# Kernel optimization log

Hardware: AMD Instinct MI355X
Metric: run time of the kernel (lower is better)

## Reference

```python
import jax, jax.numpy as jnp
import numpy as np

T, N, R = 10, 50000, 50000   # time steps, nodes per graph, total restaurants
D_IN, D, H = 128, 64, 4      # input dim, hidden dim, attention heads
E = 400000                   # edges per timestep (before self-loops)
HD = D // H                  # head dim


def setup_inputs() -> dict:
    key = jax.random.key(0)
    ks = jax.random.split(key, 16)
    inp = {}
    inp["x"] = jax.random.normal(ks[0], (T, N, D_IN), jnp.float32)
    inp["edge_index"] = jax.random.randint(ks[1], (T, 2, E), 0, N, jnp.int32)
    inp["edge_weight"] = jax.random.uniform(ks[2], (T, E), jnp.float32)
    # per-timestep permutation mapping local node idx -> global restaurant idx
    inp["global_idx"] = jax.vmap(lambda k: jax.random.permutation(k, R))(
        jax.random.split(ks[3], T)).astype(jnp.int32)
    s = 0.05
    inp["gcn1_w"] = jax.random.normal(ks[4], (D, D_IN), jnp.float32) * s
    inp["gcn1_b"] = jnp.zeros((D,), jnp.float32)
    inp["gcn2_w"] = jax.random.normal(ks[5], (D, D), jnp.float32) * s
    inp["gcn2_b"] = jnp.zeros((D,), jnp.float32)
    inp["in_proj_w"] = jax.random.normal(ks[6], (3 * D, D), jnp.float32) * s
    inp["in_proj_b"] = jnp.zeros((3 * D,), jnp.float32)
    inp["out_proj_w"] = jax.random.normal(ks[7], (D, D), jnp.float32) * s
    inp["out_proj_b"] = jnp.zeros((D,), jnp.float32)
    inp["w1"] = jnp.ones((T, D), jnp.float32)
    inp["w2"] = jnp.ones((T, D), jnp.float32)
    inp["w3"] = jnp.ones((D,), jnp.float32)
    inp["w4"] = jnp.ones((D,), jnp.float32)
    inp["ln1_g"] = jnp.ones((D,), jnp.float32)
    inp["ln1_b"] = jnp.zeros((D,), jnp.float32)
    inp["ln2_g"] = jnp.ones((D,), jnp.float32)
    inp["ln2_b"] = jnp.zeros((D,), jnp.float32)
    inp["fc_w"] = jax.random.normal(ks[8], (D, D), jnp.float32) * s
    inp["fc_b"] = jnp.zeros((D,), jnp.float32)
    return inp


def _layer_norm(x, g, b, eps=1e-5):
    mu = jnp.mean(x, axis=-1, keepdims=True)
    var = jnp.mean((x - mu) ** 2, axis=-1, keepdims=True)
    return (x - mu) * jax.lax.rsqrt(var + eps) * g + b


def _gcn_layer(h, src, dst, ew, W, b):
    # PyG GCNConv with edge weights; self-loops already appended by caller.
    deg = jax.ops.segment_sum(ew, dst, num_segments=N)
    dinv = jnp.where(deg > 0, jax.lax.rsqrt(deg), 0.0)
    norm = dinv[src] * ew * dinv[dst]                      # [E+N]
    hw = h @ W.T                                           # [N, D]
    agg = jax.ops.segment_sum(norm[:, None] * hw[src], dst, num_segments=N)
    return agg + b


def _forward(x, edge_index, edge_weight, global_idx,
             gcn1_w, gcn1_b, gcn2_w, gcn2_b,
             in_proj_w, in_proj_b, out_proj_w, out_proj_b,
             w1, w2, w3, w4, ln1_g, ln1_b, ln2_g, ln2_b, fc_w, fc_b):
    loop = jnp.arange(N, dtype=edge_index.dtype)
    src = jnp.concatenate([edge_index[:, 0], jnp.broadcast_to(loop, (T, N))], axis=1)
    dst = jnp.concatenate([edge_index[:, 1], jnp.broadcast_to(loop, (T, N))], axis=1)
    ew = jnp.concatenate([edge_weight, jnp.ones((T, N), edge_weight.dtype)], axis=1)

    def per_t(xt, st, dt, wt):
        h = jax.nn.relu(_gcn_layer(xt, st, dt, wt, gcn1_w, gcn1_b))
        return jax.nn.relu(_gcn_layer(h, st, dt, wt, gcn2_w, gcn2_b))

    feat = jax.vmap(per_t)(x, src, dst, ew)                # [T, N, D]

    # scatter local features to global alignment (permutation per timestep)
    aligned = jax.vmap(lambda g, f: jnp.zeros((R, D), f.dtype).at[g].set(f))(
        global_idx, feat)                                  # [T, R, D]
    time_embeds = jnp.transpose(aligned, (1, 0, 2))        # [R, T, D]

    presence = jax.vmap(
        lambda g: jnp.zeros((R,), bool).at[g].set(True))(global_idx)  # [T, R]
    key_padding_mask = ~presence.T                          # [R, T], True = ignore
    bias = jnp.where(key_padding_mask, -1e9, 0.0)           # [R, T]

    # multi-head self-attention over time axis (batch_first, batch = R)
    qkv = time_embeds @ in_proj_w.T + in_proj_b             # [R, T, 3D]
    q, k, v = jnp.split(qkv, 3, axis=-1)
    q = q.reshape(R, T, H, HD)
    k = k.reshape(R, T, H, HD)
    v = v.reshape(R, T, H, HD)
    scores = jnp.einsum('rthd,rshd->rhts', q, k) / np.sqrt(HD)
    scores = scores + bias[:, None, None, :]
    attn = jax.nn.softmax(scores, axis=-1)                  # [R, H, T, T]
    ao = jnp.einsum('rhts,rshd->rthd', attn, v).reshape(R, T, D)
    attn_out = ao @ out_proj_w.T + out_proj_b               # [R, T, D]

    # dropouts are identity in eval mode
    time_feat = _layer_norm(w1 * time_embeds + w2 * attn_out, ln1_g, ln1_b)
    final = time_feat[:, -1, :]                             # [R, D]
    out = final @ fc_w.T + fc_b                             # [R, D]
    return _layer_norm(w3 * final + w4 * out, ln2_g, ln2_b)


def reference(x, edge_index, edge_weight, global_idx,
              gcn1_w, gcn1_b, gcn2_w, gcn2_b,
              in_proj_w, in_proj_b, out_proj_w, out_proj_b,
              w1, w2, w3, w4, ln1_g, ln1_b, ln2_g, ln2_b, fc_w, fc_b):
    return _forward(x, edge_index, edge_weight, global_idx,
                    gcn1_w, gcn1_b, gcn2_w, gcn2_b,
                    in_proj_w, in_proj_b, out_proj_w, out_proj_b,
                    w1, w2, w3, w4, ln1_g, ln1_b, ln2_g, ln2_b, fc_w, fc_b)
```

## Files before the change

### kernel.cpp

```cpp
#include <hip/hip_runtime.h>
#include <cstdint>
#include <cstddef>

namespace {

constexpr int T = 10;
constexpr int N = 50000;
constexpr int R = 50000;
constexpr int DIN = 128;
constexpr int D = 64;
constexpr int E = 400000;

constexpr int BINS = 16384;
constexpr int NR = 4;
constexpr int SEG = 16;
constexpr int ESEG = E / SEG;
constexpr int EV4 = ESEG / 4;

constexpr float WSCALE = 262144.0f;
constexpr float WINV = 1.0f / 262144.0f;

typedef _Float16 h16;
typedef __attribute__((ext_vector_type(8))) _Float16 f16x8;
typedef __attribute__((ext_vector_type(4))) _Float16 f16x4;
typedef __attribute__((ext_vector_type(4))) float f32x4;

__global__ __launch_bounds__(256) void k_hist(const int* __restrict__ ei,
                                              const float* __restrict__ ew,
                                              unsigned* __restrict__ pu) {
  __shared__ unsigned h[BINS];
  int b = blockIdx.x;
  int s = b % SEG;
  int tr = b / SEG;
  int r = tr % NR;
  int t = tr / NR;
  for (int i = threadIdx.x; i < BINS; i += 256) h[i] = 0u;
  __syncthreads();
  int bin0 = r * BINS;
  const int4* dst4 = (const int4*)(ei + (size_t)t * 2 * E + E + s * ESEG);
  const float4* ew4 = (const float4*)(ew + (size_t)t * E + s * ESEG);
  for (int i = threadIdx.x; i < EV4; i += 256) {
    int4 d = dst4[i];
    float4 w = ew4[i];
    unsigned a0 = (unsigned)(d.x - bin0);
    unsigned a1 = (unsigned)(d.y - bin0);
    unsigned a2 = (unsigned)(d.z - bin0);
    unsigned a3 = (unsigned)(d.w - bin0);
    if (a0 < (unsigned)BINS) atomicAdd(&h[a0], 0x1000000u + (unsigned)fmaf(w.x, WSCALE, 0.5f));
    if (a1 < (unsigned)BINS) atomicAdd(&h[a1], 0x1000000u + (unsigned)fmaf(w.y, WSCALE, 0.5f));
    if (a2 < (unsigned)BINS) atomicAdd(&h[a2], 0x1000000u + (unsigned)fmaf(w.z, WSCALE, 0.5f));
    if (a3 < (unsigned)BINS) atomicAdd(&h[a3], 0x1000000u + (unsigned)fmaf(w.w, WSCALE, 0.5f));
  }
  __syncthreads();
  size_t base = (size_t)b * BINS;
  for (int i = threadIdx.x; i < BINS; i += 256) pu[base + i] = h[i];
}

__global__ __launch_bounds__(256) void k_hreduce(const unsigned* __restrict__ pu,
                                                 int* __restrict__ cnt,
                                                 float* __restrict__ dinv) {
  int i = blockIdx.x * 256 + threadIdx.x;
  if (i >= T * N) return;
  int t = i / N, n = i - t * N;
  int r = n / BINS, rel = n - r * BINS;
  unsigned c = 0;
  unsigned wsum = 0;
  #pragma unroll
  for (int s = 0; s < SEG; ++s) {
    unsigned v = pu[((size_t)((t * NR + r) * SEG + s)) * BINS + rel];
    c += v >> 24;
    wsum += v & 0xFFFFFFu;
  }
  cnt[i] = (int)c;
  dinv[i] = rsqrtf(1.0f + (float)wsum * WINV);
}

__global__ __launch_bounds__(256) void k_scan(const int* __restrict__ cnt,
                                              int* __restrict__ rowptr) {
  int t = blockIdx.x;
  int lane = threadIdx.x & 63, wid = threadIdx.x >> 6;
  __shared__ int wsum[4];
  __shared__ int carry_s;
  if (threadIdx.x == 0) carry_s = 0;
  __syncthreads();
  const int4* cp = (const int4*)(cnt + (size_t)t * N);
  int4* rp = (int4*)(rowptr + (size_t)t * N);
  constexpr int NI4 = N / 4;
  for (int base = 0; base < NI4; base += 256) {
    int i = base + threadIdx.x;
    int4 v = make_int4(0, 0, 0, 0);
    if (i < NI4) v = cp[i];
    int tot = v.x + v.y + v.z + v.w;
    int s = tot;
    #pragma unroll
    for (int off = 1; off < 64; off <<= 1) {
      int u = __shfl_up(s, off, 64);
      if (lane >= off) s += u;
    }
    if (lane == 63) wsum[wid] = s;
    int carry = carry_s;
    __syncthreads();
    int wadd = 0;
    #pragma unroll
    for (int w = 0; w < 4; ++w) if (w < wid) wadd += wsum[w];
    if (i < NI4) {
      int excl = carry + wadd + s - tot;
      int4 o;
      o.x = excl;
      o.y = excl + v.x;
      o.z = o.y + v.y;
      o.w = o.z + v.z;
      rp[i] = o;
    }
    __syncthreads();
    if (threadIdx.x == 0) carry_s = carry + wsum[0] + wsum[1] + wsum[2] + wsum[3];
    __syncthreads();
  }
}

__global__ __launch_bounds__(256) void k_segoff(unsigned* __restrict__ pu,
                                                const int* __restrict__ rowptr) {
  int i = blockIdx.x * 256 + threadIdx.x;
  if (i >= T * N) return;
  int t = i / N, n = i - t * N;
  int r = n / BINS, rel = n - r * BINS;
  unsigned run = (unsigned)rowptr[i];
  #pragma unroll
  for (int s = 0; s < SEG; ++s) {
    size_t base = ((size_t)((t * NR + r) * SEG + s)) * BINS + rel;
    unsigned v = pu[base];
    pu[base] = run;
    run += v >> 24;
  }
}

__global__ __launch_bounds__(256) void k_fill2(const int* __restrict__ ei,
                                               const float* __restrict__ ew,
                                               const unsigned* __restrict__ pu,
                                               int2* __restrict__ pk) {
  __shared__ int cur[BINS];
  int b = blockIdx.x;
  int s = b % SEG;
  int tr = b / SEG;
  int r = tr % NR;
  int t = tr / NR;
  size_t pbase = (size_t)b * BINS;
  for (int i = threadIdx.x; i < BINS; i += 256) cur[i] = (int)pu[pbase + i];
  __syncthreads();
  int bin0 = r * BINS;
  const int4* src4 = (const int4*)(ei + (size_t)t * 2 * E + s * ESEG);
  const int4* dst4 = (const int4*)(ei + (size_t)t * 2 * E + E + s * ESEG);
  const float4* ew4 = (const float4*)(ew + (size_t)t * E + s * ESEG);
  int2* pkt = pk + (size_t)t * E;
  for (int i = threadIdx.x; i < EV4; i += 256) {
    int4 d = dst4[i];
    int4 sv = src4[i];
    float4 w = ew4[i];
    unsigned a0 = (unsigned)(d.x - bin0);
    unsigned a1 = (unsigned)(d.y - bin0);
    unsigned a2 = (unsigned)(d.z - bin0);
    unsigned a3 = (unsigned)(d.w - bin0);
    if (a0 < (unsigned)BINS) {
      int pos = atomicAdd(&cur[a0], 1);
      pkt[pos] = make_int2(sv.x, __float_as_int(w.x));
    }
    if (a1 < (unsigned)BINS) {
      int pos = atomicAdd(&cur[a1], 1);
      pkt[pos] = make_int2(sv.y, __float_as_int(w.y));
    }
    if (a2 < (unsigned)BINS) {
      int pos = atomicAdd(&cur[a2], 1);
      pkt[pos] = make_int2(sv.z, __float_as_int(w.z));
    }
    if (a3 < (unsigned)BINS) {
      int pos = atomicAdd(&cur[a3], 1);
      pkt[pos] = make_int2(sv.w, __float_as_int(w.w));
    }
  }
}

__global__ __launch_bounds__(256) void k_prep(const float* __restrict__ g1w,
                                              const float* __restrict__ g2w,
                                              const float* __restrict__ inw,
                                              const float* __restrict__ outw,
                                              const float* __restrict__ fcw,
                                              h16* __restrict__ Wb) {
  int i = blockIdx.x * 256 + threadIdx.x;
  if (i >= 32768) return;
  const float* src;
  int off;
  if (i < 8192)       { src = g1w;  off = 0; }
  else if (i < 12288) { src = g2w;  off = 8192; }
  else if (i < 24576) { src = inw;  off = 12288; }
  else if (i < 28672) { src = outw; off = 24576; }
  else                { src = fcw;  off = 28672; }
  Wb[i] = (h16)src[i - off];
}

template <int K, int NT, bool F16B, int MODE>
__global__ __launch_bounds__(256) void k_mm(const h16* __restrict__ Wb,
                                            const void* __restrict__ Bv,
                                            const float* __restrict__ biasp,
                                            h16* __restrict__ out,
                                            h16* __restrict__ q9,
                                            int Mwaves) {
  int wv = threadIdx.x >> 6, lane = threadIdx.x & 63;
  int wave = blockIdx.x * 4 + wv;
  if (wave >= Mwaves) return;
  int m0 = wave * 16;
  int half = lane & 15, quad = lane >> 4;
  constexpr int KS = K / 32;
  int m = m0 + half;
  float ds = 1.0f;
  if (MODE == 2) ds = biasp[m];
  f16x8 bfrag[KS];
  if (F16B) {
    const h16* Bp = (const h16*)Bv + (size_t)m * K + quad * 8;
    #pragma unroll
    for (int ks = 0; ks < KS; ++ks) bfrag[ks] = *(const f16x8*)(Bp + ks * 32);
  } else {
    const float* Bp = (const float*)Bv + (size_t)m * K + quad * 8;
    #pragma unroll
    for (int ks = 0; ks < KS; ++ks) {
      float4 f0 = *(const float4*)(Bp + ks * 32);
      float4 f1 = *(const float4*)(Bp + ks * 32 + 4);
      f16x8 b;
      b[0] = (h16)f0.x; b[1] = (h16)f0.y; b[2] = (h16)f0.z; b[3] = (h16)f0.w;
      b[4] = (h16)f1.x; b[5] = (h16)f1.y; b[6] = (h16)f1.z; b[7] = (h16)f1.w;
      bfrag[ks] = b;
    }
  }
  #pragma unroll
  for (int jt = 0; jt < NT; ++jt) {
    f32x4 acc = {0.f, 0.f, 0.f, 0.f};
    const h16* Wp = Wb + (size_t)(jt * 16 + half) * K + quad * 8;
    #pragma unroll
    for (int ks = 0; ks < KS; ++ks) {
      f16x8 afrag = *(const f16x8*)(Wp + ks * 32);
      acc = __builtin_amdgcn_mfma_f32_16x16x32_f16(afrag, bfrag[ks], acc, 0, 0, 0);
    }
    int j = jt * 16 + quad * 4;
    if (MODE == 1) {
      float4 b4 = *(const float4*)(biasp + j);
      acc[0] += b4.x; acc[1] += b4.y; acc[2] += b4.z; acc[3] += b4.w;
    }
    if (MODE == 2) {
      acc[0] *= ds; acc[1] *= ds; acc[2] *= ds; acc[3] *= ds;
    }
    f16x4 o;
    o[0] = (h16)acc[0]; o[1] = (h16)acc[1]; o[2] = (h16)acc[2]; o[3] = (h16)acc[3];
    if (MODE != 1) {
      *(f16x4*)(out + (size_t)m * (NT * 16) + j) = o;
    } else {
      if (jt < 4) {
        if (m % 10 == 9) *(f16x4*)(q9 + (size_t)(m / 10) * 64 + j) = o;
      } else {
        *(f16x4*)(out + (size_t)m * 128 + (j - 64)) = o;
      }
    }
  }
}

template <bool SCATTER>
__global__ __launch_bounds__(256) void k_gather(
    const h16* __restrict__ hw, const int2* __restrict__ pk,
    const float* __restrict__ dinv, const int* __restrict__ rowptr,
    const int* __restrict__ cnt, const float* __restrict__ bias,
    const int* __restrict__ gidx, h16* __restrict__ outp) {
  __shared__ __align__(16) float red[4][8][68];
  int wv = threadIdx.x >> 6, lane = threadIdx.x & 63;
  int t = blockIdx.y;
  int nd = lane >> 5;
  int grp = (lane >> 3) & 3;
  int sub = lane & 7;
  int n = blockIdx.x * 8 + wv * 2 + nd;
  const h16* hwt = hw + (size_t)t * N * D;
  const int2* pkt = pk + (size_t)t * E;
  int start = rowptr[t * N + n];
  int m = cnt[t * N + n];
  int nA = blockIdx.x * 8 + wv * 2;
  int nB = nA + 1;
  float selfA = (float)hwt[(size_t)nA * D + lane];
  float selfB = (float)hwt[(size_t)nB * D + lane];
  float dnA = dinv[t * N + nA];
  float dnB = dinv[t * N + nB];
  float bi = bias[lane];
  f32x4 accL = {0.f, 0.f, 0.f, 0.f};
  f32x4 accH = {0.f, 0.f, 0.f, 0.f};
  int e = grp;
  for (; e + 4 < m; e += 8) {
    int2 ra = pkt[start + e];
    int2 rb = pkt[start + e + 4];
    float wa = __int_as_float(ra.y);
    float wb = __int_as_float(rb.y);
    f16x8 ha = *(const f16x8*)(hwt + (size_t)ra.x * D + sub * 8);
    f16x8 hb = *(const f16x8*)(hwt + (size_t)rb.x * D + sub * 8);
    #pragma unroll
    for (int j = 0; j < 4; ++j) {
      accL[j] = fmaf(wa, (float)ha[j], accL[j]);
      accH[j] = fmaf(wa, (float)ha[j + 4], accH[j]);
    }
    #pragma unroll
    for (int j = 0; j < 4; ++j) {
      accL[j] = fmaf(wb, (float)hb[j], accL[j]);
      accH[j] = fmaf(wb, (float)hb[j + 4], accH[j]);
    }
  }
  if (e < m) {
    int2 ra = pkt[start + e];
    float wa = __int_as_float(ra.y);
    f16x8 ha = *(const f16x8*)(hwt + (size_t)ra.x * D + sub * 8);
    #pragma unroll
    for (int j = 0; j < 4; ++j) {
      accL[j] = fmaf(wa, (float)ha[j], accL[j]);
      accH[j] = fmaf(wa, (float)ha[j + 4], accH[j]);
    }
  }
  float* rw = &red[wv][nd * 4 + grp][sub * 8];
  *(f32x4*)(rw) = accL;
  *(f32x4*)(rw + 4) = accH;
  __builtin_amdgcn_wave_barrier();
  #pragma unroll
  for (int d2 = 0; d2 < 2; ++d2) {
    int nn = nA + d2;
    float s = red[wv][d2 * 4 + 0][lane] + red[wv][d2 * 4 + 1][lane] +
              red[wv][d2 * 4 + 2][lane] + red[wv][d2 * 4 + 3][lane];
    float selfv = d2 ? selfB : selfA;
    float dn = d2 ? dnB : dnA;
    float v = fmaxf(fmaf(dn, s + selfv, bi), 0.f);
    size_t ro;
    if (SCATTER) {
      int rr2 = gidx[(size_t)t * R + nn];
      ro = ((size_t)rr2 * T + t) * D + lane;
    } else {
      ro = ((size_t)t * N + nn) * D + lane;
    }
    outp[ro] = (h16)v;
  }
}

__global__ __launch_bounds__(256) void k_attn2(const h16* __restrict__ kv,
                                               const h16* __restrict__ q9,
                                               h16* __restrict__ ao) {
  int wv = threadIdx.x >> 6, lane = threadIdx.x & 63;
  int r = blockIdx.x * 4 + wv;
  if (r >= R) return;
  float qv = (float)q9[(size_t)r * 64 + lane];
  const h16* kvr = kv + (size_t)r * T * 128;
  float sc[T], vv[T];
  #pragma unroll
  for (int s = 0; s < T; ++s) {
    float kk = (float)kvr[s * 128 + lane];
    vv[s] = (float)kvr[s * 128 + 64 + lane];
    float p = qv * kk;
    p += __shfl_xor(p, 8, 16);
    p += __shfl_xor(p, 4, 16);
    p += __shfl_xor(p, 2, 16);
    p += __shfl_xor(p, 1, 16);
    sc[s] = p * 0.25f;
  }
  float mx = sc[0];
  #pragma unroll
  for (int s = 1; s < T; ++s) mx = fmaxf(mx, sc[s]);
  float ssum = 0.f;
  #pragma unroll
  for (int s = 0; s < T; ++s) { sc[s] = expf(sc[s] - mx); ssum += sc[s]; }
  float rinv = 1.0f / ssum;
  float aov = 0.f;
  #pragma unroll
  for (int s = 0; s < T; ++s) aov = fmaf(sc[s] * rinv, vv[s], aov);
  ao[(size_t)r * 64 + lane] = (h16)aov;
}

__global__ __launch_bounds__(256) void k_ln1(const h16* __restrict__ te,
                                             const h16* __restrict__ proj,
                                             const float* __restrict__ outB,
                                             const float* __restrict__ w1,
                                             const float* __restrict__ w2,
                                             const float* __restrict__ g1,
                                             const float* __restrict__ b1,
                                             float* __restrict__ finf,
                                             h16* __restrict__ finb) {
  int wv = threadIdx.x >> 6, lane = threadIdx.x & 63;
  int r = blockIdx.x * 4 + wv;
  if (r >= R) return;
  float t9 = (float)te[((size_t)r * T + (T - 1)) * 64 + lane];
  float pr = (float)proj[(size_t)r * 64 + lane] + outB[lane];
  float pre = w1[(T - 1) * 64 + lane] * t9 + w2[(T - 1) * 64 + lane] * pr;
  float s1 = pre;
  #pragma unroll
  for (int off = 32; off >= 1; off >>= 1) s1 += __shfl_xor(s1, off, 64);
  float mu = s1 * (1.0f / 64.0f);
  float dv = pre - mu;
  float s2 = dv * dv;
  #pragma unroll
  for (int off = 32; off >= 1; off >>= 1) s2 += __shfl_xor(s2, off, 64);
  float rstd = 1.0f / sqrtf(s2 * (1.0f / 64.0f) + 1e-5f);
  float fin = dv * rstd * g1[lane] + b1[lane];
  finf[(size_t)r * 64 + lane] = fin;
  finb[(size_t)r * 64 + lane] = (h16)fin;
}

__global__ __launch_bounds__(256) void k_ln2(const float* __restrict__ finf,
                                             const h16* __restrict__ o2,
                                             const float* __restrict__ fcB,
                                             const float* __restrict__ w3,
                                             const float* __restrict__ w4,
                                             const float* __restrict__ g2,
                                             const float* __restrict__ b2,
                                             float* __restrict__ out) {
  int wv = threadIdx.x >> 6, lane = threadIdx.x & 63;
  int r = blockIdx.x * 4 + wv;
  if (r >= R) return;
  float fin = finf[(size_t)r * 64 + lane];
  float oo = (float)o2[(size_t)r * 64 + lane] + fcB[lane];
  float pre = w3[lane] * fin + w4[lane] * oo;
  float s1 = pre;
  #pragma unroll
  for (int off = 32; off >= 1; off >>= 1) s1 += __shfl_xor(s1, off, 64);
  float mu = s1 * (1.0f / 64.0f);
  float dv = pre - mu;
  float s2 = dv * dv;
  #pragma unroll
  for (int off = 32; off >= 1; off >>= 1) s2 += __shfl_xor(s2, off, 64);
  float rstd = 1.0f / sqrtf(s2 * (1.0f / 64.0f) + 1e-5f);
  out[(size_t)r * 64 + lane] = dv * rstd * g2[lane] + b2[lane];
}

}

extern "C" void kernel_launch(void* const* d_in, const int* in_sizes, int n_in,
                              void* d_out, int out_size, void* d_ws, size_t ws_size,
                              hipStream_t stream) {
  const float* x      = (const float*)d_in[0];
  const int*   ei     = (const int*)d_in[1];
  const float* ew     = (const float*)d_in[2];
  const int*   gidx   = (const int*)d_in[3];
  const float* gcn1_w = (const float*)d_in[4];
  const float* gcn1_b = (const float*)d_in[5];
  const float* gcn2_w = (const float*)d_in[6];
  const float* gcn2_b = (const float*)d_in[7];
  const float* in_w   = (const float*)d_in[8];
  const float* in_b   = (const float*)d_in[9];
  const float* out_w  = (const float*)d_in[10];
  const float* out_b  = (const float*)d_in[11];
  const float* w1     = (const float*)d_in[12];
  const float* w2     = (const float*)d_in[13];
  const float* w3     = (const float*)d_in[14];
  const float* w4     = (const float*)d_in[15];
  const float* ln1_g  = (const float*)d_in[16];
  const float* ln1_b  = (const float*)d_in[17];
  const float* ln2_g  = (const float*)d_in[18];
  const float* ln2_b  = (const float*)d_in[19];
  const float* fc_w   = (const float*)d_in[20];
  const float* fc_b   = (const float*)d_in[21];
  float* outp = (float*)d_out;

  char* ws = (char*)d_ws;
  size_t off = 0;
  auto alloc = [&](size_t bytes) {
    void* p = ws + off;
    off += (bytes + 255) & ~(size_t)255;
    return p;
  };
  h16* h1te = (h16*)alloc(sizeof(h16) * (size_t)T * N * D);
  h16* q9b  = (h16*)alloc(sizeof(h16) * (size_t)R * D);
  h16* aob  = (h16*)alloc(sizeof(h16) * (size_t)R * D);
  h16* proj = (h16*)alloc(sizeof(h16) * (size_t)R * D);
  float* finf = (float*)alloc(sizeof(float) * (size_t)R * D);
  h16* finb = (h16*)alloc(sizeof(h16) * (size_t)R * D);
  h16* o2b  = (h16*)alloc(sizeof(h16) * (size_t)R * D);
  h16* Wb   = (h16*)alloc(sizeof(h16) * 32768);
  size_t u_base = off;
  float* dinv   = (float*)alloc(sizeof(float) * T * N);
  int*   cnt    = (int*)alloc(sizeof(int) * T * N);
  int*   rowptr = (int*)alloc(sizeof(int) * T * N);
  int2*  pk     = (int2*)alloc(sizeof(int2) * (size_t)T * E);
  size_t pu_off = off;
  unsigned* pu  = (unsigned*)alloc(sizeof(unsigned) * (size_t)T * NR * SEG * BINS);
  h16* hw = (h16*)(ws + pu_off);
  size_t hw_end = pu_off + sizeof(h16) * (size_t)T * N * D;
  if (hw_end > off) off = hw_end;
  h16* kv = (h16*)(ws + u_base);
  size_t kv_end = u_base + sizeof(h16) * (size_t)T * N * 128;
  if (kv_end > off) off = kv_end;

  const h16* W1b = Wb;
  const h16* W2b = Wb + 8192;
  const h16* WIb = Wb + 12288;
  const h16* WOb = Wb + 24576;
  const h16* WFb = Wb + 28672;

  const int M = T * N;
  const int MW = M / 16;
  const int RW = R / 16;
  const int PREP_BLOCKS = T * NR * SEG;

  k_hist<<<PREP_BLOCKS, 256, 0, stream>>>(ei, ew, pu);
  k_hreduce<<<(T * N + 255) / 256, 256, 0, stream>>>(pu, cnt, dinv);
  k_scan<<<T, 256, 0, stream>>>(cnt, rowptr);
  k_segoff<<<(T * N + 255) / 256, 256, 0, stream>>>(pu, rowptr);
  k_fill2<<<PREP_BLOCKS, 256, 0, stream>>>(ei, ew, pu, pk);
  k_prep<<<128, 256, 0, stream>>>(gcn1_w, gcn2_w, in_w, out_w, fc_w, Wb);

  dim3 gg(N / 8, T);
  k_mm<DIN, 4, false, 2><<<(MW + 3) / 4, 256, 0, stream>>>(W1b, x, dinv, hw, nullptr, MW);
  k_gather<false><<<gg, 256, 0, stream>>>(hw, pk, dinv, rowptr, cnt, gcn1_b, nullptr, h1te);
  k_mm<D, 4, true, 2><<<(MW + 3) / 4, 256, 0, stream>>>(W2b, h1te, dinv, hw, nullptr, MW);
  k_gather<true><<<gg, 256, 0, stream>>>(hw, pk, dinv, rowptr, cnt, gcn2_b, gidx, h1te);

  k_mm<D, 12, true, 1><<<(MW + 3) / 4, 256, 0, stream>>>(WIb, h1te, in_b, kv, q9b, MW);
  k_attn2<<<(R + 3) / 4, 256, 0, stream>>>(kv, q9b, aob);
  k_mm<D, 4, true, 0><<<(RW + 3) / 4, 256, 0, stream>>>(WOb, aob, nullptr, proj, nullptr, RW);
  k_ln1<<<(R + 3) / 4, 256, 0, stream>>>(h1te, proj, out_b, w1, w2, ln1_g, ln1_b, finf, finb);
  k_mm<D, 4, true, 0><<<(RW + 3) / 4, 256, 0, stream>>>(WFb, finb, nullptr, o2b, nullptr, RW);
  k_ln2<<<(R + 3) / 4, 256, 0, stream>>>(finf, o2b, fc_b, w3, w4, ln2_g, ln2_b, outp);
}
```

Measured before the change: 1.077 ms.

## Fuse QKV projection, attention, out-proj, both LayerNorms and FC into one tail kernel

Replaces six tail kernels (QKV GEMM, attention, out-proj GEMM, LN1, FC GEMM, LN2) with a single kernel. Each block processes 16 restaurants, keeping K/V, Q, attention output and intermediate activations in LDS instead of round-tripping them through global memory. This removes the large kv intermediate write and read plus several launches. The cost is heavy LDS use per block, which may limit occupancy, and several block-wide barriers. Separately, the histogram segment count SEG is raised from 16 to 25, which changes the preprocessing grid size.

```diff
diff --git a/kernel.cpp b/kernel.cpp
--- a/kernel.cpp
+++ b/kernel.cpp
@@ -13,7 +13,7 @@
 
 constexpr int BINS = 16384;
 constexpr int NR = 4;
-constexpr int SEG = 16;
+constexpr int SEG = 25;
 constexpr int ESEG = E / SEG;
 constexpr int EV4 = ESEG / 4;
 
@@ -202,7 +202,6 @@
                                             const void* __restrict__ Bv,
                                             const float* __restrict__ biasp,
                                             h16* __restrict__ out,
-                                            h16* __restrict__ q9,
                                             int Mwaves) {
   int wv = threadIdx.x >> 6, lane = threadIdx.x & 63;
   int wave = blockIdx.x * 4 + wv;
@@ -240,24 +239,12 @@
       acc = __builtin_amdgcn_mfma_f32_16x16x32_f16(afrag, bfrag[ks], acc, 0, 0, 0);
     }
     int j = jt * 16 + quad * 4;
-    if (MODE == 1) {
-      float4 b4 = *(const float4*)(biasp + j);
-      acc[0] += b4.x; acc[1] += b4.y; acc[2] += b4.z; acc[3] += b4.w;
-    }
     if (MODE == 2) {
       acc[0] *= ds; acc[1] *= ds; acc[2] *= ds; acc[3] *= ds;
     }
     f16x4 o;
     o[0] = (h16)acc[0]; o[1] = (h16)acc[1]; o[2] = (h16)acc[2]; o[3] = (h16)acc[3];
-    if (MODE != 1) {
-      *(f16x4*)(out + (size_t)m * (NT * 16) + j) = o;
-    } else {
-      if (jt < 4) {
-        if (m % 10 == 9) *(f16x4*)(q9 + (size_t)(m / 10) * 64 + j) = o;
-      } else {
-        *(f16x4*)(out + (size_t)m * 128 + (j - 64)) = o;
-      }
-    }
+    *(f16x4*)(out + (size_t)m * (NT * 16) + j) = o;
   }
 }
 
@@ -339,92 +326,173 @@
   }
 }
 
-__global__ __launch_bounds__(256) void k_attn2(const h16* __restrict__ kv,
-                                               const h16* __restrict__ q9,
-                                               h16* __restrict__ ao) {
+constexpr int KVP = 132;
+constexpr int P72 = 72;
+
+__global__ __launch_bounds__(256) void k_tail(
+    const h16* __restrict__ te,
+    const h16* __restrict__ WIb,
+    const float* __restrict__ inB,
+    const h16* __restrict__ WOb,
+    const float* __restrict__ outB,
+    const h16* __restrict__ WFb,
+    const float* __restrict__ fcB,
+    const float* __restrict__ w1,
+    const float* __restrict__ w2,
+    const float* __restrict__ w3,
+    const float* __restrict__ w4,
+    const float* __restrict__ g1, const float* __restrict__ b1,
+    const float* __restrict__ g2, const float* __restrict__ b2,
+    float* __restrict__ outp) {
+  __shared__ __align__(16) h16 kvl[160][KVP];
+  __shared__ __align__(16) h16 ql[16][P72];
+  __shared__ __align__(16) h16 aol[16][P72];
+  __shared__ __align__(16) h16 tbuf[16][P72];
+  __shared__ __align__(16) h16 fbuf[16][P72];
+  __shared__ __align__(16) float pf[16][64];
+
   int wv = threadIdx.x >> 6, lane = threadIdx.x & 63;
-  int r = blockIdx.x * 4 + wv;
-  if (r >= R) return;
-  float qv = (float)q9[(size_t)r * 64 + lane];
-  const h16* kvr = kv + (size_t)r * T * 128;
-  float sc[T], vv[T];
+  int half = lane & 15, quad = lane >> 4;
+  int g0 = blockIdx.x * 160;
+
+  for (int tt = wv; tt < 10; tt += 4) {
+    int lr = tt * 16 + half;
+    const h16* Bp = te + (size_t)(g0 + lr) * 64 + quad * 8;
+    f16x8 b0 = *(const f16x8*)(Bp);
+    f16x8 b1f = *(const f16x8*)(Bp + 32);
+    int rloc = lr / 10;
+    bool isq = (lr - rloc * 10) == 9;
+    #pragma unroll
+    for (int jt = 0; jt < 12; ++jt) {
+      f32x4 acc = {0.f, 0.f, 0.f, 0.f};
+      const h16* Wp = WIb + (size_t)(jt * 16 + half) * 64 + quad * 8;
+      acc = __builtin_amdgcn_mfma_f32_16x16x32_f16(*(const f16x8*)(Wp), b0, acc, 0, 0, 0);
+      acc = __builtin_amdgcn_mfma_f32_16x16x32_f16(*(const f16x8*)(Wp + 32), b1f, acc, 0, 0, 0);
+      int j = jt * 16 + quad * 4;
+      float4 b4 = *(const float4*)(inB + j);
+      f16x4 o;
+      o[0] = (h16)(acc[0] + b4.x); o[1] = (h16)(acc[1] + b4.y);
+      o[2] = (h16)(acc[2] + b4.z); o[3] = (h16)(acc[3] + b4.w);
+      if (jt < 4) {
+        if (isq) *(f16x4*)(&ql[rloc][j]) = o;
+      } else {
+        *(f16x4*)(&kvl[lr][j - 64]) = o;
+      }
+    }
+  }
+  __syncthreads();
+
   #pragma unroll
-  for (int s = 0; s < T; ++s) {
-    float kk = (float)kvr[s * 128 + lane];
-    vv[s] = (float)kvr[s * 128 + 64 + lane];
-    float p = qv * kk;
-    p += __shfl_xor(p, 8, 16);
-    p += __shfl_xor(p, 4, 16);
-    p += __shfl_xor(p, 2, 16);
-    p += __shfl_xor(p, 1, 16);
-    sc[s] = p * 0.25f;
-  }
-  float mx = sc[0];
-  #pragma unroll
-  for (int s = 1; s < T; ++s) mx = fmaxf(mx, sc[s]);
-  float ssum = 0.f;
-  #pragma unroll
-  for (int s = 0; s < T; ++s) { sc[s] = expf(sc[s] - mx); ssum += sc[s]; }
-  float rinv = 1.0f / ssum;
-  float aov = 0.f;
-  #pragma unroll
-  for (int s = 0; s < T; ++s) aov = fmaf(sc[s] * rinv, vv[s], aov);
-  ao[(size_t)r * 64 + lane] = (h16)aov;
-}
-
-__global__ __launch_bounds__(256) void k_ln1(const h16* __restrict__ te,
-                                             const h16* __restrict__ proj,
-                                             const float* __restrict__ outB,
-                                             const float* __restrict__ w1,
-                                             const float* __restrict__ w2,
-                                             const float* __restrict__ g1,
-                                             const float* __restrict__ b1,
-                                             float* __restrict__ finf,
-                                             h16* __restrict__ finb) {
-  int wv = threadIdx.x >> 6, lane = threadIdx.x & 63;
-  int r = blockIdx.x * 4 + wv;
-  if (r >= R) return;
-  float t9 = (float)te[((size_t)r * T + (T - 1)) * 64 + lane];
-  float pr = (float)proj[(size_t)r * 64 + lane] + outB[lane];
-  float pre = w1[(T - 1) * 64 + lane] * t9 + w2[(T - 1) * 64 + lane] * pr;
-  float s1 = pre;
-  #pragma unroll
-  for (int off = 32; off >= 1; off >>= 1) s1 += __shfl_xor(s1, off, 64);
-  float mu = s1 * (1.0f / 64.0f);
-  float dv = pre - mu;
-  float s2 = dv * dv;
-  #pragma unroll
-  for (int off = 32; off >= 1; off >>= 1) s2 += __shfl_xor(s2, off, 64);
-  float rstd = 1.0f / sqrtf(s2 * (1.0f / 64.0f) + 1e-5f);
-  float fin = dv * rstd * g1[lane] + b1[lane];
-  finf[(size_t)r * 64 + lane] = fin;
-  finb[(size_t)r * 64 + lane] = (h16)fin;
-}
-
-__global__ __launch_bounds__(256) void k_ln2(const float* __restrict__ finf,
-                                             const h16* __restrict__ o2,
-                                             const float* __restrict__ fcB,
-                                             const float* __restrict__ w3,
-                                             const float* __restrict__ w4,
-                                             const float* __restrict__ g2,
-                                             const float* __restrict__ b2,
-                                             float* __restrict__ out) {
-  int wv = threadIdx.x >> 6, lane = threadIdx.x & 63;
-  int r = blockIdx.x * 4 + wv;
-  if (r >= R) return;
-  float fin = finf[(size_t)r * 64 + lane];
-  float oo = (float)o2[(size_t)r * 64 + lane] + fcB[lane];
-  float pre = w3[lane] * fin + w4[lane] * oo;
-  float s1 = pre;
-  #pragma unroll
-  for (int off = 32; off >= 1; off >>= 1) s1 += __shfl_xor(s1, off, 64);
-  float mu = s1 * (1.0f / 64.0f);
-  float dv = pre - mu;
-  float s2 = dv * dv;
-  #pragma unroll
-  for (int off = 32; off >= 1; off >>= 1) s2 += __shfl_xor(s2, off, 64);
-  float rstd = 1.0f / sqrtf(s2 * (1.0f / 64.0f) + 1e-5f);
-  out[(size_t)r * 64 + lane] = dv * rstd * g2[lane] + b2[lane];
+  for (int i = 0; i < 4; ++i) {
+    int rl = wv * 4 + i;
+    float qv = (float)ql[rl][lane];
+    float sc[T], vv[T];
+    #pragma unroll
+    for (int s = 0; s < T; ++s) {
+      float kk = (float)kvl[rl * 10 + s][lane];
+      vv[s] = (float)kvl[rl * 10 + s][64 + lane];
+      float p = qv * kk;
+      p += __shfl_xor(p, 8, 16);
+      p += __shfl_xor(p, 4, 16);
+      p += __shfl_xor(p, 2, 16);
+      p += __shfl_xor(p, 1, 16);
+      sc[s] = p * 0.25f;
+    }
+    float mx = sc[0];
+    #pragma unroll
+    for (int s = 1; s < T; ++s) mx = fmaxf(mx, sc[s]);
+    float ssum = 0.f;
+    #pragma unroll
+    for (int s = 0; s < T; ++s) { sc[s] = expf(sc[s] - mx); ssum += sc[s]; }
+    float rinv = 1.0f / ssum;
+    float aov = 0.f;
+    #pragma unroll
+    for (int s = 0; s < T; ++s) aov = fmaf(sc[s] * rinv, vv[s], aov);
+    aol[rl][lane] = (h16)aov;
+  }
+  __syncthreads();
+
+  {
+    const h16* Bp = &aol[half][quad * 8];
+    f16x8 b0 = *(const f16x8*)(Bp);
+    f16x8 b1f = *(const f16x8*)(Bp + 32);
+    f32x4 acc = {0.f, 0.f, 0.f, 0.f};
+    const h16* Wp = WOb + (size_t)(wv * 16 + half) * 64 + quad * 8;
+    acc = __builtin_amdgcn_mfma_f32_16x16x32_f16(*(const f16x8*)(Wp), b0, acc, 0, 0, 0);
+    acc = __builtin_amdgcn_mfma_f32_16x16x32_f16(*(const f16x8*)(Wp + 32), b1f, acc, 0, 0, 0);
+    int j = wv * 16 + quad * 4;
+    float4 b4 = *(const float4*)(outB + j);
+    f16x4 o;
+    o[0] = (h16)(acc[0] + b4.x); o[1] = (h16)(acc[1] + b4.y);
+    o[2] = (h16)(acc[2] + b4.z); o[3] = (h16)(acc[3] + b4.w);
+    *(f16x4*)(&tbuf[half][j]) = o;
+  }
+  __syncthreads();
+
+  {
+    float w1l = w1[(T - 1) * 64 + lane];
+    float w2l = w2[(T - 1) * 64 + lane];
+    float g1l = g1[lane], b1l = b1[lane];
+    #pragma unroll
+    for (int i = 0; i < 4; ++i) {
+      int rl = wv * 4 + i;
+      float t9 = (float)te[(size_t)(g0 + rl * 10 + 9) * 64 + lane];
+      float pr = (float)tbuf[rl][lane];
+      float pre = w1l * t9 + w2l * pr;
+      float s1 = pre;
+      #pragma unroll
+      for (int off = 32; off >= 1; off >>= 1) s1 += __shfl_xor(s1, off, 64);
+      float mu = s1 * (1.0f / 64.0f);
+      float dv = pre - mu;
+      float s2 = dv * dv;
+      #pragma unroll
+      for (int off = 32; off >= 1; off >>= 1) s2 += __shfl_xor(s2, off, 64);
+      float rstd = 1.0f / sqrtf(s2 * (1.0f / 64.0f) + 1e-5f);
+      float fin = dv * rstd * g1l + b1l;
+      pf[rl][lane] = fin;
+      fbuf[rl][lane] = (h16)fin;
+    }
+  }
+  __syncthreads();
+
+  {
+    const h16* Bp = &fbuf[half][quad * 8];
+    f16x8 b0 = *(const f16x8*)(Bp);
+    f16x8 b1f = *(const f16x8*)(Bp + 32);
+    f32x4 acc = {0.f, 0.f, 0.f, 0.f};
+    const h16* Wp = WFb + (size_t)(wv * 16 + half) * 64 + quad * 8;
+    acc = __builtin_amdgcn_mfma_f32_16x16x32_f16(*(const f16x8*)(Wp), b0, acc, 0, 0, 0);
+    acc = __builtin_amdgcn_mfma_f32_16x16x32_f16(*(const f16x8*)(Wp + 32), b1f, acc, 0, 0, 0);
+    int j = wv * 16 + quad * 4;
+    float4 b4 = *(const float4*)(fcB + j);
+    f16x4 o;
+    o[0] = (h16)(acc[0] + b4.x); o[1] = (h16)(acc[1] + b4.y);
+    o[2] = (h16)(acc[2] + b4.z); o[3] = (h16)(acc[3] + b4.w);
+    *(f16x4*)(&tbuf[half][j]) = o;
+  }
+  __syncthreads();
+
+  {
+    float w3l = w3[lane], w4l = w4[lane];
+    float g2l = g2[lane], b2l = b2[lane];
+    #pragma unroll
+    for (int i = 0; i < 4; ++i) {
+      int rl = wv * 4 + i;
+      float fin = pf[rl][lane];
+      float oo = (float)tbuf[rl][lane];
+      float pre = w3l * fin + w4l * oo;
+      float s1 = pre;
+      #pragma unroll
+      for (int off = 32; off >= 1; off >>= 1) s1 += __shfl_xor(s1, off, 64);
+      float mu = s1 * (1.0f / 64.0f);
+      float dv = pre - mu;
+      float s2 = dv * dv;
+      #pragma unroll
+      for (int off = 32; off >= 1; off >>= 1) s2 += __shfl_xor(s2, off, 64);
+      float rstd = 1.0f / sqrtf(s2 * (1.0f / 64.0f) + 1e-5f);
+      outp[(size_t)(blockIdx.x * 16 + rl) * 64 + lane] = dv * rstd * g2l + b2l;
+    }
+  }
 }
 
 }
@@ -464,14 +532,7 @@
     return p;
   };
   h16* h1te = (h16*)alloc(sizeof(h16) * (size_t)T * N * D);
-  h16* q9b  = (h16*)alloc(sizeof(h16) * (size_t)R * D);
-  h16* aob  = (h16*)alloc(sizeof(h16) * (size_t)R * D);
-  h16* proj = (h16*)alloc(sizeof(h16) * (size_t)R * D);
-  float* finf = (float*)alloc(sizeof(float) * (size_t)R * D);
-  h16* finb = (h16*)alloc(sizeof(h16) * (size_t)R * D);
-  h16* o2b  = (h16*)alloc(sizeof(h16) * (size_t)R * D);
   h16* Wb   = (h16*)alloc(sizeof(h16) * 32768);
-  size_t u_base = off;
   float* dinv   = (float*)alloc(sizeof(float) * T * N);
   int*   cnt    = (int*)alloc(sizeof(int) * T * N);
   int*   rowptr = (int*)alloc(sizeof(int) * T * N);
@@ -481,9 +542,6 @@
   h16* hw = (h16*)(ws + pu_off);
   size_t hw_end = pu_off + sizeof(h16) * (size_t)T * N * D;
   if (hw_end > off) off = hw_end;
-  h16* kv = (h16*)(ws + u_base);
-  size_t kv_end = u_base + sizeof(h16) * (size_t)T * N * 128;
-  if (kv_end > off) off = kv_end;
 
   const h16* W1b = Wb;
   const h16* W2b = Wb + 8192;
@@ -493,7 +551,6 @@
 
   const int M = T * N;
   const int MW = M / 16;
-  const int RW = R / 16;
   const int PREP_BLOCKS = T * NR * SEG;
 
   k_hist<<<PREP_BLOCKS, 256, 0, stream>>>(ei, ew, pu);
@@ -504,15 +561,11 @@
   k_prep<<<128, 256, 0, stream>>>(gcn1_w, gcn2_w, in_w, out_w, fc_w, Wb);
 
   dim3 gg(N / 8, T);
-  k_mm<DIN, 4, false, 2><<<(MW + 3) / 4, 256, 0, stream>>>(W1b, x, dinv, hw, nullptr, MW);
+  k_mm<DIN, 4, false, 2><<<(MW + 3) / 4, 256, 0, stream>>>(W1b, x, dinv, hw, MW);
   k_gather<false><<<gg, 256, 0, stream>>>(hw, pk, dinv, rowptr, cnt, gcn1_b, nullptr, h1te);
-  k_mm<D, 4, true, 2><<<(MW + 3) / 4, 256, 0, stream>>>(W2b, h1te, dinv, hw, nullptr, MW);
+  k_mm<D, 4, true, 2><<<(MW + 3) / 4, 256, 0, stream>>>(W2b, h1te, dinv, hw, MW);
   k_gather<true><<<gg, 256, 0, stream>>>(hw, pk, dinv, rowptr, cnt, gcn2_b, gidx, h1te);
 
-  k_mm<D, 12, true, 1><<<(MW + 3) / 4, 256, 0, stream>>>(WIb, h1te, in_b, kv, q9b, MW);
-  k_attn2<<<(R + 3) / 4, 256, 0, stream>>>(kv, q9b, aob);
-  k_mm<D, 4, true, 0><<<(RW + 3) / 4, 256, 0, stream>>>(WOb, aob, nullptr, proj, nullptr, RW);
-  k_ln1<<<(R + 3) / 4, 256, 0, stream>>>(h1te, proj, out_b, w1, w2, ln1_g, ln1_b, finf, finb);
-  k_mm<D, 4, true, 0><<<(RW + 3) / 4, 256, 0, stream>>>(WFb, finb, nullptr, o2b, nullptr, RW);
-  k_ln2<<<(R + 3) / 4, 256, 0, stream>>>(finf, o2b, fc_b, w3, w4, ln2_g, ln2_b, outp);
-}
+  k_tail<<<R / 16, 256, 0, stream>>>(h1te, WIb, in_b, WOb, out_b, WFb, fc_b,
+                                     w1, w2, w3, w4, ln1_g, ln1_b, ln2_g, ln2_b, outp);
+}
```

Measured after the change: 985.7 us. 1.09x faster.
